# Optimization experiments

Hardware: AMD Instinct MI355X
Metric: run time of the kernel (lower is better)

Reference implementation:

```python
import jax, jax.numpy as jnp
import numpy as np

N, E, F, H = 50000, 800000, 64, 4
NEG_SLOPE = 0.2
LN_EPS = 1e-5


def setup_inputs() -> dict:
    key = jax.random.key(0)
    ks = jax.random.split(key, 12)
    h = jax.random.normal(ks[0], (N, F), dtype=jnp.float32)
    src = jax.random.randint(ks[1], (E,), 0, N, dtype=jnp.int32)
    dst = jax.random.randint(ks[2], (E,), 0, N, dtype=jnp.int32)
    s = 1.0 / np.sqrt(F)
    fc_w = jax.random.uniform(ks[3], (F, H * F), jnp.float32, -s, s)
    attn_l = jax.random.normal(ks[4], (H, F), dtype=jnp.float32) * s
    attn_r = jax.random.normal(ks[5], (H, F), dtype=jnp.float32) * s
    gat_bias = jnp.zeros((H * F,), dtype=jnp.float32)
    so = 1.0 / np.sqrt(H * F)
    out_w = jax.random.uniform(ks[6], (H * F, F), jnp.float32, -so, so)
    out_b = jax.random.uniform(ks[7], (F,), jnp.float32, -so, so)
    ln_g = jnp.ones((F,), dtype=jnp.float32)
    ln_b = jnp.zeros((F,), dtype=jnp.float32)
    return {"h": h, "src": src, "dst": dst, "fc_w": fc_w, "attn_l": attn_l,
            "attn_r": attn_r, "gat_bias": gat_bias, "out_w": out_w,
            "out_b": out_b, "ln_g": ln_g, "ln_b": ln_b}


def reference(h, src, dst, fc_w, attn_l, attn_r, gat_bias, out_w, out_b, ln_g, ln_b):
    # --- GATConv (DGL semantics) ---
    feat = (h @ fc_w).reshape(N, H, F)                      # [N,H,F]
    el = jnp.einsum('nhf,hf->nh', feat, attn_l)             # [N,H]
    er = jnp.einsum('nhf,hf->nh', feat, attn_r)             # [N,H]
    e = jax.nn.leaky_relu(el[src] + er[dst], NEG_SLOPE)     # [E,H]
    # edge softmax over incoming edges of each dst node
    m = jax.ops.segment_max(e, dst, num_segments=N)         # [N,H]
    ex = jnp.exp(e - m[dst])                                # [E,H]
    z = jax.ops.segment_sum(ex, dst, num_segments=N)        # [N,H]
    alpha = ex / z[dst]                                     # [E,H]
    msg = feat[src] * alpha[:, :, None]                     # [E,H,F]
    rst = jax.ops.segment_sum(msg, dst, num_segments=N)     # [N,H,F]
    rst = rst + gat_bias.reshape(H, F)
    # --- out linear + layernorm ---
    x = rst.reshape(N, H * F) @ out_w + out_b               # [N,F]
    mu = jnp.mean(x, axis=-1, keepdims=True)
    var = jnp.var(x, axis=-1, keepdims=True)
    return (x - mu) * jax.lax.rsqrt(var + LN_EPS) * ln_g + ln_b
```

## Files before the change

### kernel.cpp

```cpp
#include <hip/hip_runtime.h>

#define NN 50000
#define EE 800000
#define FF 64
#define HH 4
#define HF 256
#define NEG_SLOPE 0.2f
#define LN_EPS 1e-5f
#define WPACK_N (4 * 8 * 64 * 8)
#define NTILE (NN / 16)
#define TROW 264
#define NXCD 8
#define RCAP 48

typedef __attribute__((ext_vector_type(8))) short s8v;
typedef __attribute__((ext_vector_type(4))) float f4v;

__device__ __forceinline__ unsigned short f32_to_bf16_rne(float x) {
  unsigned int u = __float_as_uint(x);
  unsigned int r = u + 0x7FFFu + ((u >> 16) & 1u);
  return (unsigned short)(r >> 16);
}

__device__ __forceinline__ float readlane_f(float v, int l) {
  return __uint_as_float(
      (unsigned)__builtin_amdgcn_readlane((int)__float_as_uint(v), l));
}

__global__ __launch_bounds__(256) void k_prep(
    const float* __restrict__ fc_w, const float* __restrict__ out_w,
    const float* __restrict__ attn_l, const float* __restrict__ attn_r,
    const float* __restrict__ gat_bias, const float* __restrict__ out_b,
    unsigned short* __restrict__ wpack, float* __restrict__ alv,
    float* __restrict__ arv, float* __restrict__ outb2,
    int* __restrict__ cnt8) {
  const int idx = blockIdx.x * 256 + threadIdx.x;
  if (idx < WPACK_N) {
    const int j = idx & 7;
    const int l = (idx >> 3) & 63;
    const int t = (idx >> 9) & 7;
    const int ct = idx >> 12;
    const int k = 32 * t + (l >> 4) * 8 + j;
    const int c = 16 * ct + (l & 15);
    const int hh = k >> 6, kk = k & 63;
    const float* fw = fc_w + kk * HF + hh * FF;
    const float* ow = out_w + (size_t)(hh * FF) * FF + c;
    float acc = 0.f;
#pragma unroll
    for (int ff = 0; ff < FF; ++ff) acc = fmaf(fw[ff], ow[(size_t)ff * FF], acc);
    wpack[idx] = f32_to_bf16_rne(acc);
  } else if (idx < WPACK_N + 512) {
    const int i = idx - WPACK_N;
    const int hh = (i >> 6) & 3, kk = i & 63;
    const float* fw = fc_w + kk * HF + hh * FF;
    const float* at = (i < 256 ? attn_l : attn_r) + hh * FF;
    float acc = 0.f;
#pragma unroll
    for (int ff = 0; ff < FF; ++ff) acc = fmaf(fw[ff], at[ff], acc);
    (i < 256 ? alv : arv)[(hh << 6) | kk] = acc;
  } else if (idx < WPACK_N + 512 + FF) {
    const int c = idx - WPACK_N - 512;
    float acc = out_b[c];
    for (int k = 0; k < HF; ++k) acc = fmaf(gat_bias[k], out_w[(size_t)k * FF + c], acc);
    outb2[c] = acc;
  }
  if (idx < NXCD * NN) cnt8[idx] = 0;
}

__global__ __launch_bounds__(256) void k_elr(
    const float* __restrict__ h, const float* __restrict__ alv,
    const float* __restrict__ arv, unsigned short* __restrict__ hb,
    float* __restrict__ el, float* __restrict__ er) {
  const int wave = threadIdx.x >> 6;
  const int lane = threadIdx.x & 63;
  const int row = blockIdx.x * 32 + wave * 8 + (lane >> 3);
  if (row >= NN) return;
  const int kc = (lane & 7) * 8;

  float hv[8];
  *(float4*)hv = *(const float4*)(h + (size_t)row * FF + kc);
  *(float4*)(hv + 4) = *(const float4*)(h + (size_t)row * FF + kc + 4);

  unsigned pk[4];
#pragma unroll
  for (int jj = 0; jj < 4; ++jj)
    pk[jj] = (unsigned)f32_to_bf16_rne(hv[2 * jj]) |
             ((unsigned)f32_to_bf16_rne(hv[2 * jj + 1]) << 16);
  *(uint4*)(hb + (size_t)row * FF + kc) = make_uint4(pk[0], pk[1], pk[2], pk[3]);

  float p[8];
#pragma unroll
  for (int hh = 0; hh < 4; ++hh) {
    const float* av = alv + (hh << 6) + kc;
    const float* bv = arv + (hh << 6) + kc;
    float sa = 0.f, sb = 0.f;
#pragma unroll
    for (int j = 0; j < 8; ++j) {
      sa = fmaf(hv[j], av[j], sa);
      sb = fmaf(hv[j], bv[j], sb);
    }
    p[hh] = sa; p[4 + hh] = sb;
  }
#pragma unroll
  for (int off = 1; off < 8; off <<= 1) {
#pragma unroll
    for (int q = 0; q < 8; ++q) p[q] += __shfl_xor(p[q], off, 64);
  }
  const int q = lane & 7;
  if (q < 4) el[(size_t)row * 4 + q] = p[q];
  else       er[(size_t)row * 4 + (q - 4)] = p[q];
}

__global__ __launch_bounds__(256) void k_scatter(
    const int* __restrict__ src, const int* __restrict__ dst,
    int* __restrict__ cnt8, unsigned short* __restrict__ colp8) {
  unsigned xcd;
  asm("s_getreg_b32 %0, hwreg(HW_REG_XCC_ID)" : "=s"(xcd));
  xcd &= 7;
  const int e = blockIdx.x * 256 + threadIdx.x;
  if (e < EE) {
    const int d = dst[e];
    const int sv = src[e];
    const int pos = __hip_atomic_fetch_add(&cnt8[xcd * NN + d], 1,
                                           __ATOMIC_RELAXED,
                                           __HIP_MEMORY_SCOPE_WORKGROUP);
    if (pos < RCAP)
      colp8[((size_t)xcd * NN + d) * RCAP + pos] = (unsigned short)sv;
  }
}

__global__ __launch_bounds__(256) void k_gather_out(
    const unsigned short* __restrict__ hb, const float* __restrict__ el,
    const float* __restrict__ er, const int* __restrict__ cnt8,
    const unsigned short* __restrict__ colp8,
    const unsigned short* __restrict__ wpack, const float* __restrict__ outb2,
    const float* __restrict__ ln_g, const float* __restrict__ ln_b,
    float* __restrict__ out) {
  __shared__ unsigned short tile[16][TROW];
  __shared__ float part[4][16][2];
  const int wave = threadIdx.x >> 6;
  const int lane = threadIdx.x & 63;
  const int n0 = blockIdx.x * 16;
  const int nbase = n0 + wave * 4;

  int cgrp = 0;
  if (lane < 32) cgrp = cnt8[(lane >> 2) * NN + nbase + (lane & 3)];
  cgrp = cgrp > RCAP ? RCAP : cgrp;
  int inc = cgrp;
#pragma unroll
  for (int off = 4; off <= 16; off <<= 1) {
    const int t = __shfl_up(inc, off, 64);
    if (lane >= off) inc += t;
  }
  const int exc = inc - cgrp;

#pragma unroll
  for (int r = 0; r < 4; ++r) {
    const int row = wave * 4 + r;
    const int n = nbase + r;
    const float4 erv = *(const float4*)(er + (size_t)n * 4);

    const int mi = __builtin_amdgcn_readlane(inc, 28 + r);
    const int m = mi > 64 ? 64 : mi;
    const int p1 = __builtin_amdgcn_readlane(exc, 4 + r);
    const int p2 = __builtin_amdgcn_readlane(exc, 8 + r);
    const int p3 = __builtin_amdgcn_readlane(exc, 12 + r);
    const int p4 = __builtin_amdgcn_readlane(exc, 16 + r);
    const int p5 = __builtin_amdgcn_readlane(exc, 20 + r);
    const int p6 = __builtin_amdgcn_readlane(exc, 24 + r);
    const int p7 = __builtin_amdgcn_readlane(exc, 28 + r);
    int seg = 0, pb = 0;
    if (lane >= p1) { seg = 1; pb = p1; }
    if (lane >= p2) { seg = 2; pb = p2; }
    if (lane >= p3) { seg = 3; pb = p3; }
    if (lane >= p4) { seg = 4; pb = p4; }
    if (lane >= p5) { seg = 5; pb = p5; }
    if (lane >= p6) { seg = 6; pb = p6; }
    if (lane >= p7) { seg = 7; pb = p7; }
    int s = 0;
    if (lane < m)
      s = colp8[((size_t)seg * NN + n) * RCAP + (lane - pb)];

    float w0 = 0.f, w1 = 0.f, w2 = 0.f, w3 = 0.f;
    if (lane < m) {
      const float4 elv = *(const float4*)(el + (size_t)s * 4);
      float e0 = elv.x + erv.x, e1 = elv.y + erv.y;
      float e2 = elv.z + erv.z, e3 = elv.w + erv.w;
      e0 = e0 > 0.f ? e0 : NEG_SLOPE * e0;
      e1 = e1 > 0.f ? e1 : NEG_SLOPE * e1;
      e2 = e2 > 0.f ? e2 : NEG_SLOPE * e2;
      e3 = e3 > 0.f ? e3 : NEG_SLOPE * e3;
      w0 = __expf(e0); w1 = __expf(e1);
      w2 = __expf(e2); w3 = __expf(e3);
    }
    float z0 = w0, z1 = w1, z2 = w2, z3 = w3;
#pragma unroll
    for (int off = 1; off < 64; off <<= 1) {
      z0 += __shfl_xor(z0, off, 64);
      z1 += __shfl_xor(z1, off, 64);
      z2 += __shfl_xor(z2, off, 64);
      z3 += __shfl_xor(z3, off, 64);
    }
    w0 *= (z0 > 0.f ? 1.f / z0 : 0.f);
    w1 *= (z1 > 0.f ? 1.f / z1 : 0.f);
    w2 *= (z2 > 0.f ? 1.f / z2 : 0.f);
    w3 *= (z3 > 0.f ? 1.f / z3 : 0.f);

    float a0 = 0.f, a1 = 0.f, a2 = 0.f, a3 = 0.f;
    for (int e = 0; e < m; e += 8) {
#pragma unroll
      for (int j = 0; j < 8; ++j) {
        const int le = e + j;
        const int se = __builtin_amdgcn_readlane(s, le);
        const unsigned short* rowp = hb + ((unsigned)se << 6);
        const float xv = __uint_as_float((unsigned)rowp[lane] << 16);
        const float we0 = readlane_f(w0, le);
        const float we1 = readlane_f(w1, le);
        const float we2 = readlane_f(w2, le);
        const float we3 = readlane_f(w3, le);
        a0 = fmaf(we0, xv, a0);
        a1 = fmaf(we1, xv, a1);
        a2 = fmaf(we2, xv, a2);
        a3 = fmaf(we3, xv, a3);
      }
    }
    tile[row][lane]       = f32_to_bf16_rne(a0);
    tile[row][64 + lane]  = f32_to_bf16_rne(a1);
    tile[row][128 + lane] = f32_to_bf16_rne(a2);
    tile[row][192 + lane] = f32_to_bf16_rne(a3);
  }
  __syncthreads();

  const int cl = lane & 15;
  const int quad = lane >> 4;
  s8v a[8];
#pragma unroll
  for (int t = 0; t < 8; ++t)
    a[t] = *(const s8v*)(&tile[cl][32 * t + quad * 8]);

  f4v acc = {0.f, 0.f, 0.f, 0.f};
#pragma unroll
  for (int t = 0; t < 8; ++t) {
    const s8v b = *(const s8v*)(wpack + ((wave * 8 + t) * 64 + lane) * 8);
    acc = __builtin_amdgcn_mfma_f32_16x16x32_bf16(a[t], b, acc, 0, 0, 0);
  }

  const float ob = outb2[16 * wave + cl];
  float xv[4];
#pragma unroll
  for (int r = 0; r < 4; ++r) {
    const float v = acc[r] + ob;
    xv[r] = v;
    float p1 = v, p2 = v * v;
#pragma unroll
    for (int off = 1; off < 16; off <<= 1) {
      p1 += __shfl_xor(p1, off, 64);
      p2 += __shfl_xor(p2, off, 64);
    }
    if (cl == 0) {
      part[wave][quad * 4 + r][0] = p1;
      part[wave][quad * 4 + r][1] = p2;
    }
  }
  __syncthreads();
#pragma unroll
  for (int r = 0; r < 4; ++r) {
    const int row = quad * 4 + r;
    const float t1 = part[0][row][0] + part[1][row][0] +
                     part[2][row][0] + part[3][row][0];
    const float t2 = part[0][row][1] + part[1][row][1] +
                     part[2][row][1] + part[3][row][1];
    const float mu = t1 * (1.f / 64.f);
    const float var = t2 * (1.f / 64.f) - mu * mu;
    const float inv = rsqrtf(var + LN_EPS);
    const int c = 16 * wave + cl;
    out[(size_t)(n0 + row) * FF + c] = (xv[r] - mu) * inv * ln_g[c] + ln_b[c];
  }
}

extern "C" void kernel_launch(void* const* d_in, const int* in_sizes, int n_in,
                              void* d_out, int out_size, void* d_ws,
                              size_t ws_size, hipStream_t stream) {
  const float* h_in   = (const float*)d_in[0];
  const int*   src    = (const int*)d_in[1];
  const int*   dst    = (const int*)d_in[2];
  const float* fc_w   = (const float*)d_in[3];
  const float* attn_l = (const float*)d_in[4];
  const float* attn_r = (const float*)d_in[5];
  const float* gbias  = (const float*)d_in[6];
  const float* out_w  = (const float*)d_in[7];
  const float* out_b  = (const float*)d_in[8];
  const float* ln_g   = (const float*)d_in[9];
  const float* ln_b   = (const float*)d_in[10];
  float* out = (float*)d_out;

  char* p = (char*)d_ws;
  auto alloc = [&](size_t bytes) {
    char* q = p;
    p += (bytes + 255) & ~(size_t)255;
    return q;
  };
  unsigned short* hb     = (unsigned short*)alloc((size_t)NN * FF * 2);
  unsigned short* wpack  = (unsigned short*)alloc((size_t)WPACK_N * 2);
  float* alv     = (float*)alloc(256 * 4);
  float* arv     = (float*)alloc(256 * 4);
  float* outb2   = (float*)alloc(64 * 4);
  float* el      = (float*)alloc((size_t)NN * HH * 4);
  float* er      = (float*)alloc((size_t)NN * HH * 4);
  int*   cnt8    = (int*)alloc((size_t)NXCD * NN * 4);
  unsigned short* colp8 =
      (unsigned short*)alloc((size_t)NXCD * NN * RCAP * 2);

  k_prep<<<(NXCD * NN + 255) / 256, 256, 0, stream>>>(
      fc_w, out_w, attn_l, attn_r, gbias, out_b, wpack, alv, arv, outb2, cnt8);
  k_elr<<<(NN + 31) / 32, 256, 0, stream>>>(h_in, alv, arv, hb, el, er);
  k_scatter<<<(EE + 255) / 256, 256, 0, stream>>>(src, dst, cnt8, colp8);
  k_gather_out<<<NTILE, 256, 0, stream>>>(hb, el, er, cnt8, colp8, wpack,
                                          outb2, ln_g, ln_b, out);
}
```

Measured before the change: 192.3 us.

## Compute per-node attention aggregation with bf16 MFMA instead of scalar readlane FMAs

Replaces the per-edge scalar loop (readlane of weights plus four FMAs per edge) with staging of neighbor feature rows and attention weights into LDS, then a 16x16x32 bf16 MFMA per 32-edge chunk. It always processes 32 edge slots (64 if the degree exceeds 32), relying on zeroed weights for padded slots. This trades extra LDS traffic, unconditional gathers of padded rows, and bf16 rounding of the attention weights for fewer VALU and readlane instructions.

```diff
diff --git a/kernel.cpp b/kernel.cpp
--- a/kernel.cpp
+++ b/kernel.cpp
@@ -20,11 +20,6 @@
   unsigned int u = __float_as_uint(x);
   unsigned int r = u + 0x7FFFu + ((u >> 16) & 1u);
   return (unsigned short)(r >> 16);
-}
-
-__device__ __forceinline__ float readlane_f(float v, int l) {
-  return __uint_as_float(
-      (unsigned)__builtin_amdgcn_readlane((int)__float_as_uint(v), l));
 }
 
 __global__ __launch_bounds__(256) void k_prep(
@@ -138,10 +133,13 @@
     float* __restrict__ out) {
   __shared__ unsigned short tile[16][TROW];
   __shared__ float part[4][16][2];
+  __shared__ unsigned short xa[4][2560];
   const int wave = threadIdx.x >> 6;
   const int lane = threadIdx.x & 63;
   const int n0 = blockIdx.x * 16;
   const int nbase = n0 + wave * 4;
+  unsigned short* Xw = &xa[wave][0];
+  unsigned short* Aw = &xa[wave][2048];
 
   int cgrp = 0;
   if (lane < 32) cgrp = cnt8[(lane >> 2) * NN + nbase + (lane & 3)];
@@ -206,28 +204,81 @@
     w2 *= (z2 > 0.f ? 1.f / z2 : 0.f);
     w3 *= (z3 > 0.f ? 1.f / z3 : 0.f);
 
-    float a0 = 0.f, a1 = 0.f, a2 = 0.f, a3 = 0.f;
-    for (int e = 0; e < m; e += 8) {
-#pragma unroll
-      for (int j = 0; j < 8; ++j) {
-        const int le = e + j;
-        const int se = __builtin_amdgcn_readlane(s, le);
-        const unsigned short* rowp = hb + ((unsigned)se << 6);
-        const float xv = __uint_as_float((unsigned)rowp[lane] << 16);
-        const float we0 = readlane_f(w0, le);
-        const float we1 = readlane_f(w1, le);
-        const float we2 = readlane_f(w2, le);
-        const float we3 = readlane_f(w3, le);
-        a0 = fmaf(we0, xv, a0);
-        a1 = fmaf(we1, xv, a1);
-        a2 = fmaf(we2, xv, a2);
-        a3 = fmaf(we3, xv, a3);
+    if (lane < 32) {
+      const int ai = ((lane >> 3) << 7) | (lane & 7);
+      Aw[ai]      = f32_to_bf16_rne(w0);
+      Aw[ai + 32] = f32_to_bf16_rne(w1);
+      Aw[ai + 64] = f32_to_bf16_rne(w2);
+      Aw[ai + 96] = f32_to_bf16_rne(w3);
+    }
+
+#pragma unroll
+    for (int e = 0; e < 32; e += 8) {
+      unsigned short t0, t1, t2, t3, t4, t5, t6, t7;
+      t0 = hb[((unsigned)__builtin_amdgcn_readlane(s, e + 0) << 6) + lane];
+      t1 = hb[((unsigned)__builtin_amdgcn_readlane(s, e + 1) << 6) + lane];
+      t2 = hb[((unsigned)__builtin_amdgcn_readlane(s, e + 2) << 6) + lane];
+      t3 = hb[((unsigned)__builtin_amdgcn_readlane(s, e + 3) << 6) + lane];
+      t4 = hb[((unsigned)__builtin_amdgcn_readlane(s, e + 4) << 6) + lane];
+      t5 = hb[((unsigned)__builtin_amdgcn_readlane(s, e + 5) << 6) + lane];
+      t6 = hb[((unsigned)__builtin_amdgcn_readlane(s, e + 6) << 6) + lane];
+      t7 = hb[((unsigned)__builtin_amdgcn_readlane(s, e + 7) << 6) + lane];
+      const unsigned u0 = (unsigned)t0 | ((unsigned)t1 << 16);
+      const unsigned u1 = (unsigned)t2 | ((unsigned)t3 << 16);
+      const unsigned u2 = (unsigned)t4 | ((unsigned)t5 << 16);
+      const unsigned u3 = (unsigned)t6 | ((unsigned)t7 << 16);
+      *(uint4*)(Xw + (e << 6) + (lane << 3)) = make_uint4(u0, u1, u2, u3);
+    }
+
+    const s8v af = *(const s8v*)(Aw + (((lane >> 4) << 7) | ((lane & 15) << 3)));
+    f4v acc[4];
+#pragma unroll
+    for (int ct = 0; ct < 4; ++ct) {
+      const f4v z4 = {0.f, 0.f, 0.f, 0.f};
+      const s8v bf = *(const s8v*)(
+          Xw + (((lane >> 4) << 9) | (((ct << 4) | (lane & 15)) << 3)));
+      acc[ct] = __builtin_amdgcn_mfma_f32_16x16x32_bf16(af, bf, z4, 0, 0, 0);
+    }
+
+    if (m > 32) {
+      if (lane >= 32) {
+        const int e2 = lane - 32;
+        const int ai = ((e2 >> 3) << 7) | (e2 & 7);
+        Aw[ai]      = f32_to_bf16_rne(w0);
+        Aw[ai + 32] = f32_to_bf16_rne(w1);
+        Aw[ai + 64] = f32_to_bf16_rne(w2);
+        Aw[ai + 96] = f32_to_bf16_rne(w3);
       }
-    }
-    tile[row][lane]       = f32_to_bf16_rne(a0);
-    tile[row][64 + lane]  = f32_to_bf16_rne(a1);
-    tile[row][128 + lane] = f32_to_bf16_rne(a2);
-    tile[row][192 + lane] = f32_to_bf16_rne(a3);
+#pragma unroll
+      for (int e = 32; e < 64; e += 8) {
+        unsigned short t0, t1, t2, t3, t4, t5, t6, t7;
+        t0 = hb[((unsigned)__builtin_amdgcn_readlane(s, e + 0) << 6) + lane];
+        t1 = hb[((unsigned)__builtin_amdgcn_readlane(s, e + 1) << 6) + lane];
+        t2 = hb[((unsigned)__builtin_amdgcn_readlane(s, e + 2) << 6) + lane];
+        t3 = hb[((unsigned)__builtin_amdgcn_readlane(s, e + 3) << 6) + lane];
+        t4 = hb[((unsigned)__builtin_amdgcn_readlane(s, e + 4) << 6) + lane];
+        t5 = hb[((unsigned)__builtin_amdgcn_readlane(s, e + 5) << 6) + lane];
+        t6 = hb[((unsigned)__builtin_amdgcn_readlane(s, e + 6) << 6) + lane];
+        t7 = hb[((unsigned)__builtin_amdgcn_readlane(s, e + 7) << 6) + lane];
+        const unsigned u0 = (unsigned)t0 | ((unsigned)t1 << 16);
+        const unsigned u1 = (unsigned)t2 | ((unsigned)t3 << 16);
+        const unsigned u2 = (unsigned)t4 | ((unsigned)t5 << 16);
+        const unsigned u3 = (unsigned)t6 | ((unsigned)t7 << 16);
+        *(uint4*)(Xw + ((e - 32) << 6) + (lane << 3)) = make_uint4(u0, u1, u2, u3);
+      }
+      const s8v af2 = *(const s8v*)(Aw + (((lane >> 4) << 7) | ((lane & 15) << 3)));
+#pragma unroll
+      for (int ct = 0; ct < 4; ++ct) {
+        const s8v bf = *(const s8v*)(
+            Xw + (((lane >> 4) << 9) | (((ct << 4) | (lane & 15)) << 3)));
+        acc[ct] = __builtin_amdgcn_mfma_f32_16x16x32_bf16(af2, bf, acc[ct], 0, 0, 0);
+      }
+    }
+
+    const int q = lane >> 4, r2 = lane & 15;
+#pragma unroll
+    for (int ct = 0; ct < 4; ++ct)
+      tile[row][(q << 6) | (ct << 4) | r2] = f32_to_bf16_rne(acc[ct][0]);
   }
   __syncthreads();
 
```

Measured after the change: 183.9 us. 1.05x faster.
